# Performance work log

Hardware: AMD Instinct MI355X
Metric: run time of the kernel (lower is better)

Reference implementation:

```python
import jax, jax.numpy as jnp
import numpy as np

N_NODES = 32768
N_EDGES = 524288
IN_CH = 128
OUT_CH = 128
EDGE_CH = 64
HIDDEN = 128


def setup_inputs() -> dict:
    key = jax.random.key(0)
    ks = jax.random.split(key, 8)
    x = jax.random.normal(ks[0], (N_NODES, IN_CH), dtype=jnp.float32)
    edge_index = jax.random.randint(ks[1], (2, N_EDGES), 0, N_NODES, dtype=jnp.int64)
    edge_attr = jax.random.uniform(ks[2], (N_EDGES, EDGE_CH), dtype=jnp.float32)
    # filter_network: Linear(edge_ch, hidden) -> tanh -> Linear(hidden, out)
    s1 = 1.0 / np.sqrt(EDGE_CH)
    s2 = 1.0 / np.sqrt(HIDDEN)
    W1 = jax.random.uniform(ks[3], (EDGE_CH, HIDDEN), jnp.float32, -s1, s1)
    b1 = jax.random.uniform(ks[4], (HIDDEN,), jnp.float32, -s1, s1)
    W2 = jax.random.uniform(ks[5], (HIDDEN, OUT_CH), jnp.float32, -s2, s2)
    b2 = jax.random.uniform(ks[6], (OUT_CH,), jnp.float32, -s2, s2)
    # attention_vector [out, 1], xavier_uniform with gain 1.414
    lim = 1.414 * np.sqrt(6.0 / (OUT_CH + 1))
    attn = jax.random.uniform(ks[7], (OUT_CH,), jnp.float32, -lim, lim)
    return {"x": x, "edge_index": edge_index, "edge_attr": edge_attr,
            "W1": W1, "b1": b1, "W2": W2, "b2": b2, "attn": attn}


def _segment_softmax(scores, segment_ids, num_segments):
    # PyG-style numerically stable softmax over segments
    seg_max = jax.ops.segment_max(scores, segment_ids, num_segments=num_segments)
    seg_max = jnp.where(jnp.isfinite(seg_max), seg_max, 0.0)
    e = jnp.exp(scores - seg_max[segment_ids])
    denom = jax.ops.segment_sum(e, segment_ids, num_segments=num_segments)
    return e / (denom[segment_ids] + 1e-16)


def reference(x, edge_index, edge_attr, W1, b1, W2, b2, attn):
    source, target = edge_index[0], edge_index[1]
    n_nodes = x.shape[0]
    source_features = x[source]                                  # [E, in]
    edge_attr_norm = edge_attr / (jnp.linalg.norm(edge_attr, axis=-1, keepdims=True) + 1e-8)
    h = jnp.tanh(edge_attr_norm @ W1 + b1)                       # [E, hidden]
    edge_filters = h @ W2 + b2                                   # [E, out]
    messages = source_features * edge_filters                    # [E, out]
    attention_scores = messages @ attn                           # [E]
    attention_weights = _segment_softmax(attention_scores, target, n_nodes)
    messages = messages * attention_weights[:, None]
    output = jax.ops.segment_sum(messages, target, num_segments=n_nodes)  # [N, out]
    return output, attention_weights
```

## Files before the change

### kernel.cpp

```cpp
#include <hip/hip_runtime.h>
#include <stdint.h>

typedef short short8 __attribute__((ext_vector_type(8)));
typedef float f32x16 __attribute__((ext_vector_type(16)));
typedef unsigned ux4 __attribute__((ext_vector_type(4)));

__device__ __forceinline__ unsigned cvtpk(float lo, float hi){
  unsigned r;
  asm("v_cvt_pk_bf16_f32 %0, %1, %2" : "=v"(r) : "v"(lo), "v"(hi));
  return r;
}

__device__ __forceinline__ short8 frag_from(unsigned a, unsigned b, unsigned c, unsigned d){
  union { unsigned u[4]; short8 s; } t;
  t.u[0] = a; t.u[1] = b; t.u[2] = c; t.u[3] = d;
  return t.s;
}

__global__ void k_setup(const float* __restrict__ x, uint2* __restrict__ xb, int n4,
                        const int* __restrict__ ei, int* __restrict__ rowptr, int E,
                        const float* __restrict__ W1, const float* __restrict__ W2,
                        ux4* __restrict__ Wf)
{
  const long long tid = (long long)blockIdx.x * 256 + threadIdx.x;
  if (tid < 48 * 64) {
    const int f = (int)(tid >> 6), l = (int)(tid & 63);
    const int r = l & 31, hh = l >> 5;
    float v[8];
    if (f < 16) {
      const int mf = f >> 2, ks = f & 3;
      const int c = 32 * mf + r, kb = ks * 16 + hh * 8;
#pragma unroll
      for (int j = 0; j < 8; ++j) v[j] = W1[(kb + j) * 128 + c];
    } else {
      const int f2 = f - 16, mf2 = f2 >> 3, ks = f2 & 7;
      const int o = 32 * mf2 + r, cb = ks * 16 + hh * 8;
#pragma unroll
      for (int j = 0; j < 8; ++j) v[j] = W2[(cb + j) * 128 + o];
    }
    ux4 d;
    d.x = cvtpk(v[0], v[1]); d.y = cvtpk(v[2], v[3]);
    d.z = cvtpk(v[4], v[5]); d.w = cvtpk(v[6], v[7]);
    Wf[(long long)f * 64 + l] = d;
  }
  const long long tot = (n4 > E) ? n4 : E;
  for (long long i = tid; i < tot; i += (long long)gridDim.x * 256) {
    if (i < n4) {
      float4 v = ((const float4*)x)[i];
      uint2 o; o.x = cvtpk(v.x, v.y); o.y = cvtpk(v.z, v.w);
      xb[i] = o;
    }
    if (i < E) atomicAdd(&rowptr[ei[E + i]], 1);
  }
}

__global__ __launch_bounds__(1024)
void k_scan(int* __restrict__ p, int N){
  __shared__ int ls[1024];
  const int t = threadIdx.x;
  const int chunk = (N + 1023) >> 10;
  const int c0 = t * chunk, c1 = min(N, c0 + chunk);
  int s = 0;
  for (int i = c0; i < c1; ++i) s += p[i];
  ls[t] = s;
  __syncthreads();
  for (int off = 1; off < 1024; off <<= 1) {
    int add = (t >= off) ? ls[t - off] : 0;
    __syncthreads();
    ls[t] += add;
    __syncthreads();
  }
  int run = (t == 0) ? 0 : ls[t - 1];
  for (int i = c0; i < c1; ++i) { int v = p[i]; p[i] = run; run += v; }
}

__global__ void k_fill(const int* __restrict__ ei, int* __restrict__ rowptr,
                       int* __restrict__ pose, int* __restrict__ eidx, int E){
  for (long long i = (long long)blockIdx.x * 256 + threadIdx.x; i < E;
       i += (long long)gridDim.x * 256) {
    int tg = ei[E + i];
    int pos = atomicAdd(&rowptr[tg], 1);
    if (pose) pose[i] = pos;
    eidx[pos] = (int)i;
  }
}

#define K1B 512
__global__ __launch_bounds__(K1B)
void k1_fused(const unsigned* __restrict__ xb, const int* __restrict__ ei,
              const float* __restrict__ ea, const ux4* __restrict__ Wf,
              const float* __restrict__ b1, const float* __restrict__ b2,
              const float* __restrict__ attn, const int* __restrict__ eidx,
              unsigned* __restrict__ msgp, float* __restrict__ scoreS, int E)
{
  __shared__ ux4 sWf[48 * 64];
  for (int i = threadIdx.x; i < 48 * 64; i += K1B) sWf[i] = Wf[i];
  __syncthreads();

  const int lane = threadIdx.x & 63;
  const int wv   = threadIdx.x >> 6;
  const int h    = lane >> 5;
  const int r31  = lane & 31;
  const long long gstep = (long long)gridDim.x * (K1B / 64) * 32;
  long long p = ((long long)blockIdx.x * (K1B / 64) + wv) * 32 + r31;
  if (p - r31 >= E) return;

  int eC = eidx[(p < E) ? p : (long long)(E - 1)];
  int srcC = ei[eC];
  unsigned ebC[4][4]; float rinC;
  {
    const float* er = ea + (long long)eC * 64 + h * 8;
    float4 v[8];
#pragma unroll
    for (int ks = 0; ks < 4; ++ks) {
      v[2*ks]   = *(const float4*)(er + ks * 16);
      v[2*ks+1] = *(const float4*)(er + ks * 16 + 4);
    }
    float ss = 0.f;
#pragma unroll
    for (int k8 = 0; k8 < 8; ++k8) {
      ss = fmaf(v[k8].x, v[k8].x, ss); ss = fmaf(v[k8].y, v[k8].y, ss);
      ss = fmaf(v[k8].z, v[k8].z, ss); ss = fmaf(v[k8].w, v[k8].w, ss);
    }
    ss += __shfl_xor(ss, 32);
    rinC = 1.0f / (sqrtf(ss) + 1e-8f);
#pragma unroll
    for (int ks = 0; ks < 4; ++ks) {
      ebC[ks][0] = cvtpk(v[2*ks].x,   v[2*ks].y);
      ebC[ks][1] = cvtpk(v[2*ks].z,   v[2*ks].w);
      ebC[ks][2] = cvtpk(v[2*ks+1].x, v[2*ks+1].y);
      ebC[ks][3] = cvtpk(v[2*ks+1].z, v[2*ks+1].w);
    }
  }
  long long pn = p + gstep;
  bool hasN = (pn - r31) < E;
  int eN = 0;
  if (hasN) eN = eidx[(pn < E) ? pn : (long long)(E - 1)];

  while (true) {
    float4 eaN[8]; int srcN = 0;
    if (hasN) {
      srcN = ei[eN];
      const float* er = ea + (long long)eN * 64 + h * 8;
#pragma unroll
      for (int ks = 0; ks < 4; ++ks) {
        eaN[2*ks]   = *(const float4*)(er + ks * 16);
        eaN[2*ks+1] = *(const float4*)(er + ks * 16 + 4);
      }
    }
    long long pnn = pn + gstep;
    bool hasNN = hasN && ((pnn - r31) < E);
    int eNN = 0;
    if (hasNN) eNN = eidx[(pnn < E) ? pnn : (long long)(E - 1)];

    const unsigned* xrow = xb + (long long)srcC * 64;
    uint2 xw[4];
#pragma unroll
    for (int rq = 0; rq < 4; ++rq)
      xw[rq] = *(const uint2*)(xrow + (8*rq + 4*h) / 2);
    asm volatile("" ::: "memory");

    unsigned hb[8][4];
#pragma unroll
    for (int mf = 0; mf < 4; ++mf) {
      f32x16 a1;
#pragma unroll
      for (int i = 0; i < 16; ++i) a1[i] = 0.f;
#pragma unroll
      for (int ks = 0; ks < 4; ++ks) {
        ux4 w = sWf[(mf * 4 + ks) * 64 + lane];
        a1 = __builtin_amdgcn_mfma_f32_32x32x16_bf16(
            frag_from(w.x, w.y, w.z, w.w),
            frag_from(ebC[ks][0], ebC[ks][1], ebC[ks][2], ebC[ks][3]), a1, 0, 0, 0);
      }
      float hv[16];
#pragma unroll
      for (int rq = 0; rq < 4; ++rq) {
        float4 bc = *(const float4*)(b1 + 32*mf + 8*rq + 4*h);
#pragma unroll
        for (int i = 0; i < 4; ++i) {
          float pre = fmaf(a1[rq*4+i], rinC, ((const float*)&bc)[i]);
          float e2  = __expf(2.0f * pre);
          hv[rq*4+i] = 1.0f - 2.0f / (e2 + 1.0f);
        }
      }
#pragma unroll
      for (int q = 0; q < 2; ++q) {
        unsigned A = cvtpk(hv[q*8+0], hv[q*8+1]);
        unsigned B = cvtpk(hv[q*8+2], hv[q*8+3]);
        unsigned C = cvtpk(hv[q*8+4], hv[q*8+5]);
        unsigned D = cvtpk(hv[q*8+6], hv[q*8+7]);
        unsigned Axr = (unsigned)__shfl_xor((int)A, 32);
        unsigned Bxr = (unsigned)__shfl_xor((int)B, 32);
        unsigned Cxr = (unsigned)__shfl_xor((int)C, 32);
        unsigned Dxr = (unsigned)__shfl_xor((int)D, 32);
        hb[2*mf+q][0] = h ? Cxr : A;
        hb[2*mf+q][1] = h ? Dxr : B;
        hb[2*mf+q][2] = h ? C   : Axr;
        hb[2*mf+q][3] = h ? D   : Bxr;
      }
    }

    float score = 0.f;
#pragma unroll
    for (int mf2 = 0; mf2 < 4; ++mf2) {
      uint2 xwN[4];
      if (mf2 < 3) {
#pragma unroll
        for (int rq = 0; rq < 4; ++rq)
          xwN[rq] = *(const uint2*)(xrow + (32*(mf2+1) + 8*rq + 4*h) / 2);
      }
      f32x16 a2;
#pragma unroll
      for (int i = 0; i < 16; ++i) a2[i] = 0.f;
#pragma unroll
      for (int ks = 0; ks < 8; ++ks) {
        ux4 w = sWf[(16 + mf2 * 8 + ks) * 64 + lane];
        a2 = __builtin_amdgcn_mfma_f32_32x32x16_bf16(
            frag_from(w.x, w.y, w.z, w.w),
            frag_from(hb[ks][0], hb[ks][1], hb[ks][2], hb[ks][3]), a2, 0, 0, 0);
      }
      unsigned pk[8];
#pragma unroll
      for (int rq = 0; rq < 4; ++rq) {
        const int o0 = 32*mf2 + 8*rq + 4*h;
        float4 b2c = *(const float4*)(b2 + o0);
        float4 atc = *(const float4*)(attn + o0);
        float x0 = __uint_as_float(xw[rq].x << 16);
        float x1 = __uint_as_float(xw[rq].x & 0xffff0000u);
        float x2 = __uint_as_float(xw[rq].y << 16);
        float x3 = __uint_as_float(xw[rq].y & 0xffff0000u);
        float m0 = (a2[rq*4+0] + b2c.x) * x0;
        float m1 = (a2[rq*4+1] + b2c.y) * x1;
        float m2 = (a2[rq*4+2] + b2c.z) * x2;
        float m3 = (a2[rq*4+3] + b2c.w) * x3;
        score = fmaf(m0, atc.x, score);
        score = fmaf(m1, atc.y, score);
        score = fmaf(m2, atc.z, score);
        score = fmaf(m3, atc.w, score);
        pk[2*rq]   = cvtpk(m0, m1);
        pk[2*rq+1] = cvtpk(m2, m3);
      }
      if (p < E) {
        ux4* dst = (ux4*)(msgp + p * 64 + 16*mf2 + 8*h);
        ux4 s0, s1;
        s0.x = pk[0]; s0.y = pk[1]; s0.z = pk[2]; s0.w = pk[3];
        s1.x = pk[4]; s1.y = pk[5]; s1.z = pk[6]; s1.w = pk[7];
        dst[0] = s0; dst[1] = s1;
      }
      if (mf2 < 3) {
#pragma unroll
        for (int rq = 0; rq < 4; ++rq) xw[rq] = xwN[rq];
      }
    }
    score += __shfl_xor(score, 32);
    if (h == 0 && p < E) scoreS[p] = score;

    if (!hasN) break;
    float ss = 0.f;
#pragma unroll
    for (int k8 = 0; k8 < 8; ++k8) {
      ss = fmaf(eaN[k8].x, eaN[k8].x, ss); ss = fmaf(eaN[k8].y, eaN[k8].y, ss);
      ss = fmaf(eaN[k8].z, eaN[k8].z, ss); ss = fmaf(eaN[k8].w, eaN[k8].w, ss);
    }
    ss += __shfl_xor(ss, 32);
    rinC = 1.0f / (sqrtf(ss) + 1e-8f);
#pragma unroll
    for (int ks = 0; ks < 4; ++ks) {
      ebC[ks][0] = cvtpk(eaN[2*ks].x,   eaN[2*ks].y);
      ebC[ks][1] = cvtpk(eaN[2*ks].z,   eaN[2*ks].w);
      ebC[ks][2] = cvtpk(eaN[2*ks+1].x, eaN[2*ks+1].y);
      ebC[ks][3] = cvtpk(eaN[2*ks+1].z, eaN[2*ks+1].w);
    }
    srcC = srcN; p = pn; pn = pnn; hasN = hasNN; eN = eNN;
  }
}

template<int FUSEW>
__global__ __launch_bounds__(256)
void k_gather(const unsigned* __restrict__ msgp, const float* __restrict__ scoreS,
              const int* __restrict__ rowptr, const int* __restrict__ eidx,
              float* __restrict__ lse, float* __restrict__ wreg,
              float* __restrict__ out, int N)
{
  const int lane = threadIdx.x & 63;
  const int node = blockIdx.x * 4 + (threadIdx.x >> 6);
  if (node >= N) return;
  const int end   = rowptr[node];
  const int start = node ? rowptr[node - 1] : 0;
  const int L     = end - start;

  if (L <= 64) {
    float sc = (lane < L) ? scoreS[start + lane] : -3.4e38f;
    float mn = sc;
#pragma unroll
    for (int off = 32; off; off >>= 1) mn = fmaxf(mn, __shfl_xor(mn, off));
    float ex = (lane < L) ? __expf(sc - mn) : 0.f;
    float s = ex;
#pragma unroll
    for (int off = 32; off; off >>= 1) s += __shfl_xor(s, off);
    const float w = ex / (s + 1e-16f);
    if (FUSEW) {
      if (lane < L) wreg[eidx[start + lane]] = w;
    } else if (lane == 0) {
      lse[node] = mn + logf(s + 1e-16f);
    }

    const int g = lane & 15;
    const int q = lane >> 4;
    float acc8[8];
#pragma unroll
    for (int i = 0; i < 8; ++i) acc8[i] = 0.f;
    const int nit = (L + 3) >> 2;
#pragma unroll 2
    for (int it = 0; it < nit; ++it) {
      const int r = 4 * it + q;
      const float wj = __shfl(w, r);
      ux4 md = *(const ux4*)(msgp + (long long)(start + r) * 64 + 4 * g);
#pragma unroll
      for (int k = 0; k < 4; ++k) {
        const unsigned u = ((const unsigned*)&md)[k];
        acc8[2*k]   = fmaf(wj, __uint_as_float(u << 16),          acc8[2*k]);
        acc8[2*k+1] = fmaf(wj, __uint_as_float(u & 0xffff0000u), acc8[2*k+1]);
      }
    }
#pragma unroll
    for (int i = 0; i < 8; ++i) {
      acc8[i] += __shfl_xor(acc8[i], 16);
      acc8[i] += __shfl_xor(acc8[i], 32);
    }
    if (lane < 16) {
#pragma unroll
      for (int k = 0; k < 4; ++k) {
        const int u = 4 * lane + k;
        const int ch0 = 32*(u >> 4) + 8*((u >> 1) & 3) + 4*((u >> 3) & 1) + 2*(u & 1);
        float2 o; o.x = acc8[2*k]; o.y = acc8[2*k+1];
        *(float2*)(out + (long long)node * 128 + ch0) = o;
      }
    }
    return;
  }

  float2 acc; acc.x = 0.f; acc.y = 0.f;
  float m = -3.4e38f, s = 0.f;
  for (int c0 = 0; c0 < L; c0 += 64) {
    const int j = c0 + lane;
    float sc = (j < L) ? scoreS[start + j] : -3.4e38f;
    float cm = sc;
#pragma unroll
    for (int off = 32; off; off >>= 1) cm = fmaxf(cm, __shfl_xor(cm, off));
    const float mn = fmaxf(m, cm);
    float ex = (j < L) ? __expf(sc - mn) : 0.f;
#pragma unroll
    for (int off = 32; off; off >>= 1) ex += __shfl_xor(ex, off);
    s = s * __expf(m - mn) + ex;
    m = mn;
  }
  const float lsev = m + logf(s + 1e-16f);
  if (!FUSEW && lane == 0) lse[node] = lsev;

  for (int c0 = 0; c0 < L; c0 += 64) {
    const int j = c0 + lane;
    float w = (j < L) ? __expf(scoreS[start + j] - lsev) : 0.f;
    if (FUSEW && j < L) wreg[eidx[start + j]] = w;
    const int jn = min(64, L - c0);
#pragma unroll 4
    for (int j2 = 0; j2 < jn; ++j2) {
      float wj = __shfl(w, j2);
      unsigned md = msgp[(long long)(start + c0 + j2) * 64 + lane];
      acc.x = fmaf(wj, __uint_as_float(md << 16),          acc.x);
      acc.y = fmaf(wj, __uint_as_float(md & 0xffff0000u), acc.y);
    }
  }
  const int mf2 = lane >> 4, hh = (lane >> 3) & 1, rq = (lane >> 1) & 3, half = lane & 1;
  const int ch0 = 32*mf2 + 8*rq + 4*hh + 2*half;
  *(float2*)(out + (long long)node * 128 + ch0) = acc;
}

__global__ void k_wfin(int* __restrict__ pw, const int* __restrict__ ei,
                       const float* __restrict__ scoreS, const float* __restrict__ lse,
                       int E){
  for (long long i = (long long)blockIdx.x * 256 + threadIdx.x; i < E;
       i += (long long)gridDim.x * 256) {
    int pos = pw[i];
    float w = __expf(scoreS[pos] - lse[ei[E + i]]);
    pw[i] = __float_as_int(w);
  }
}

extern "C" void kernel_launch(void* const* d_in, const int* in_sizes, int n_in,
                              void* d_out, int out_size, void* d_ws, size_t ws_size,
                              hipStream_t stream)
{
  const float* x    = (const float*)d_in[0];
  const int*   ei   = (const int*)d_in[1];
  const float* ea   = (const float*)d_in[2];
  const float* W1   = (const float*)d_in[3];
  const float* b1   = (const float*)d_in[4];
  const float* W2   = (const float*)d_in[5];
  const float* b2   = (const float*)d_in[6];
  const float* attn = (const float*)d_in[7];
  const int N = in_sizes[0] / 128;
  const int E = in_sizes[2] / 64;
  if (E <= 0 || N <= 0) return;

  float* out   = (float*)d_out;
  float* wregN = out + (long long)N * 128;
  ux4*     Wf     = (ux4*)d_out;
  size_t   offE   = 65536;
  int*     eidxDO = (int*)((char*)d_out + offE);
  size_t   offX   = (offE + (size_t)E * 4 + 255) & ~(size_t)255;
  unsigned* xb    = (unsigned*)((char*)d_out + offX);

  char* wsb = (char*)d_ws;
  unsigned* msgp   = (unsigned*)wsb;
  float*    scoreS = (float*)(wsb + (size_t)E * 256);
  int*      rowptr = (int*)(wsb + (size_t)E * 260);
  float*    lse    = (float*)(wsb + (size_t)E * 260 + (size_t)N * 4);
  int*      eidxWS = (int*)(wsb + (size_t)E * 260 + (size_t)N * 8);
  const size_t need1 = (size_t)E * 260 + (size_t)N * 8;
  const size_t need2 = need1 + (size_t)E * 4;
  if (ws_size < need1) return;
  if ((size_t)out_size < (size_t)N * 128 + (size_t)E) return;
  if ((size_t)N * 512 < offX + (size_t)N * 256) return;

  const bool fused = (ws_size >= need2);
  int* eidx = fused ? eidxWS : eidxDO;

  (void)hipMemsetAsync(rowptr, 0, (size_t)N * 4, stream);
  k_setup<<<1024, 256, 0, stream>>>(x, (uint2*)xb, N * 32, ei, rowptr, E, W1, W2, Wf);
  k_scan<<<1, 1024, 0, stream>>>(rowptr, N);
  k_fill<<<1024, 256, 0, stream>>>(ei, rowptr, fused ? nullptr : (int*)wregN, eidx, E);
  const long long nwaves = ((long long)E + 31) / 32;
  const int grid = (int)min((long long)512, (nwaves + (K1B/64) - 1) / (K1B/64));
  k1_fused<<<grid, K1B, 0, stream>>>(xb, ei, ea, Wf, b1, b2, attn,
                                     eidx, msgp, scoreS, E);
  if (fused) {
    k_gather<1><<<(N + 3) / 4, 256, 0, stream>>>(msgp, scoreS, rowptr, eidx,
                                                 lse, wregN, out, N);
  } else {
    k_gather<0><<<(N + 3) / 4, 256, 0, stream>>>(msgp, scoreS, rowptr, eidx,
                                                 lse, wregN, out, N);
    k_wfin<<<1024, 256, 0, stream>>>((int*)wregN, ei, scoreS, lse, E);
  }
}
```

Baseline: 261.4 us.

## Merge all stages into one cooperative persistent kernel with grid syncs

Replaces the memset, setup, single-block scan, fill, fused message, and gather launches with one cooperative kernel that moves between phases using grid-wide syncs. The scan becomes a two-level multi-block scan instead of one 1024-thread block, and the weight fragments are built straight into shared memory. This is meant to remove launch gaps and the serial scan bottleneck. In exchange, the grid is capped by occupancy at no more than 512 blocks, the gather phase now runs on this fixed grid instead of one block per four nodes, and host-side device-property and occupancy queries are added to every call.

```diff
diff --git a/kernel.cpp b/kernel.cpp
--- a/kernel.cpp
+++ b/kernel.cpp
@@ -1,5 +1,8 @@
 #include <hip/hip_runtime.h>
+#include <hip/hip_cooperative_groups.h>
 #include <stdint.h>
+
+namespace cg = cooperative_groups;
 
 typedef short short8 __attribute__((ext_vector_type(8)));
 typedef float f32x16 __attribute__((ext_vector_type(16)));
@@ -17,14 +20,36 @@
   return t.s;
 }
 
-__global__ void k_setup(const float* __restrict__ x, uint2* __restrict__ xb, int n4,
-                        const int* __restrict__ ei, int* __restrict__ rowptr, int E,
-                        const float* __restrict__ W1, const float* __restrict__ W2,
-                        ux4* __restrict__ Wf)
+struct SM {
+  ux4 wf[3072];
+  int scan[512];
+};
+
+#define MBLK 512
+
+__global__ __launch_bounds__(MBLK, 4)
+void k_mega(const float* __restrict__ x, const int* __restrict__ ei,
+            const float* __restrict__ ea, const float* __restrict__ W1,
+            const float* __restrict__ b1, const float* __restrict__ W2,
+            const float* __restrict__ b2, const float* __restrict__ attn,
+            unsigned* __restrict__ xb, int* __restrict__ eidx,
+            unsigned* __restrict__ msgp, float* __restrict__ scoreS,
+            int* __restrict__ rowptr, int* __restrict__ bsum,
+            float* __restrict__ wreg, float* __restrict__ out, int N, int E)
 {
-  const long long tid = (long long)blockIdx.x * 256 + threadIdx.x;
-  if (tid < 48 * 64) {
-    const int f = (int)(tid >> 6), l = (int)(tid & 63);
+  cg::grid_group g = cg::this_grid();
+  __shared__ SM sm;
+
+  const int tix  = threadIdx.x;
+  const int lane = tix & 63;
+  const int wv   = tix >> 6;
+  const int h    = lane >> 5;
+  const int r31  = lane & 31;
+  const long long gsz = (long long)gridDim.x * MBLK;
+  const long long gt  = (long long)blockIdx.x * MBLK + tix;
+
+  for (int t = tix; t < 3072; t += MBLK) {
+    const int f = t >> 6, l = t & 63;
     const int r = l & 31, hh = l >> 5;
     float v[8];
     if (f < 16) {
@@ -41,350 +66,330 @@
     ux4 d;
     d.x = cvtpk(v[0], v[1]); d.y = cvtpk(v[2], v[3]);
     d.z = cvtpk(v[4], v[5]); d.w = cvtpk(v[6], v[7]);
-    Wf[(long long)f * 64 + l] = d;
-  }
-  const long long tot = (n4 > E) ? n4 : E;
-  for (long long i = tid; i < tot; i += (long long)gridDim.x * 256) {
-    if (i < n4) {
+    sm.wf[t] = d;
+  }
+  for (long long i = gt; i < N; i += gsz) rowptr[i] = 0;
+  {
+    const long long n4 = (long long)N * 32;
+    for (long long i = gt; i < n4; i += gsz) {
       float4 v = ((const float4*)x)[i];
       uint2 o; o.x = cvtpk(v.x, v.y); o.y = cvtpk(v.z, v.w);
-      xb[i] = o;
-    }
-    if (i < E) atomicAdd(&rowptr[ei[E + i]], 1);
-  }
-}
-
-__global__ __launch_bounds__(1024)
-void k_scan(int* __restrict__ p, int N){
-  __shared__ int ls[1024];
-  const int t = threadIdx.x;
-  const int chunk = (N + 1023) >> 10;
-  const int c0 = t * chunk, c1 = min(N, c0 + chunk);
-  int s = 0;
-  for (int i = c0; i < c1; ++i) s += p[i];
-  ls[t] = s;
-  __syncthreads();
-  for (int off = 1; off < 1024; off <<= 1) {
-    int add = (t >= off) ? ls[t - off] : 0;
+      ((uint2*)xb)[i] = o;
+    }
+  }
+  g.sync();
+
+  for (long long i = gt; i < E; i += gsz)
+    atomicAdd(&rowptr[ei[E + i]], 1);
+  g.sync();
+
+  {
+    const int B   = gridDim.x;
+    const int npb = (N + B - 1) / B;
+    const int npt = (npb + MBLK - 1) / MBLK;
+    const int base = blockIdx.x * npb;
+    const int lim  = min(base + npb, N);
+    const int i0 = base + tix * npt;
+    const int i1 = min(lim, i0 + npt);
+    int s = 0;
+    for (int i = i0; i < i1; ++i) s += rowptr[i];
+    sm.scan[tix] = s;
     __syncthreads();
-    ls[t] += add;
-    __syncthreads();
-  }
-  int run = (t == 0) ? 0 : ls[t - 1];
-  for (int i = c0; i < c1; ++i) { int v = p[i]; p[i] = run; run += v; }
-}
-
-__global__ void k_fill(const int* __restrict__ ei, int* __restrict__ rowptr,
-                       int* __restrict__ pose, int* __restrict__ eidx, int E){
-  for (long long i = (long long)blockIdx.x * 256 + threadIdx.x; i < E;
-       i += (long long)gridDim.x * 256) {
+    for (int off = 1; off < MBLK; off <<= 1) {
+      int add = (tix >= off) ? sm.scan[tix - off] : 0;
+      __syncthreads();
+      sm.scan[tix] += add;
+      __syncthreads();
+    }
+    int run = tix ? sm.scan[tix - 1] : 0;
+    for (int i = i0; i < i1; ++i) { int v = rowptr[i]; rowptr[i] = run; run += v; }
+    if (tix == MBLK - 1) bsum[blockIdx.x] = sm.scan[MBLK - 1];
+    g.sync();
+    if (blockIdx.x == 0) {
+      int v = (tix < B) ? bsum[tix] : 0;
+      sm.scan[tix] = v;
+      __syncthreads();
+      for (int off = 1; off < MBLK; off <<= 1) {
+        int add = (tix >= off) ? sm.scan[tix - off] : 0;
+        __syncthreads();
+        sm.scan[tix] += add;
+        __syncthreads();
+      }
+      if (tix < B) bsum[tix] = tix ? sm.scan[tix - 1] : 0;
+    }
+    g.sync();
+    const int add = bsum[blockIdx.x];
+    if (add) for (int i = i0; i < i1; ++i) rowptr[i] += add;
+  }
+  g.sync();
+
+  for (long long i = gt; i < E; i += gsz) {
     int tg = ei[E + i];
     int pos = atomicAdd(&rowptr[tg], 1);
-    if (pose) pose[i] = pos;
     eidx[pos] = (int)i;
   }
-}
-
-#define K1B 512
-__global__ __launch_bounds__(K1B)
-void k1_fused(const unsigned* __restrict__ xb, const int* __restrict__ ei,
-              const float* __restrict__ ea, const ux4* __restrict__ Wf,
-              const float* __restrict__ b1, const float* __restrict__ b2,
-              const float* __restrict__ attn, const int* __restrict__ eidx,
-              unsigned* __restrict__ msgp, float* __restrict__ scoreS, int E)
-{
-  __shared__ ux4 sWf[48 * 64];
-  for (int i = threadIdx.x; i < 48 * 64; i += K1B) sWf[i] = Wf[i];
-  __syncthreads();
-
-  const int lane = threadIdx.x & 63;
-  const int wv   = threadIdx.x >> 6;
-  const int h    = lane >> 5;
-  const int r31  = lane & 31;
-  const long long gstep = (long long)gridDim.x * (K1B / 64) * 32;
-  long long p = ((long long)blockIdx.x * (K1B / 64) + wv) * 32 + r31;
-  if (p - r31 >= E) return;
-
-  int eC = eidx[(p < E) ? p : (long long)(E - 1)];
-  int srcC = ei[eC];
-  unsigned ebC[4][4]; float rinC;
+  g.sync();
+
   {
-    const float* er = ea + (long long)eC * 64 + h * 8;
-    float4 v[8];
-#pragma unroll
-    for (int ks = 0; ks < 4; ++ks) {
-      v[2*ks]   = *(const float4*)(er + ks * 16);
-      v[2*ks+1] = *(const float4*)(er + ks * 16 + 4);
-    }
-    float ss = 0.f;
-#pragma unroll
-    for (int k8 = 0; k8 < 8; ++k8) {
-      ss = fmaf(v[k8].x, v[k8].x, ss); ss = fmaf(v[k8].y, v[k8].y, ss);
-      ss = fmaf(v[k8].z, v[k8].z, ss); ss = fmaf(v[k8].w, v[k8].w, ss);
-    }
-    ss += __shfl_xor(ss, 32);
-    rinC = 1.0f / (sqrtf(ss) + 1e-8f);
-#pragma unroll
-    for (int ks = 0; ks < 4; ++ks) {
-      ebC[ks][0] = cvtpk(v[2*ks].x,   v[2*ks].y);
-      ebC[ks][1] = cvtpk(v[2*ks].z,   v[2*ks].w);
-      ebC[ks][2] = cvtpk(v[2*ks+1].x, v[2*ks+1].y);
-      ebC[ks][3] = cvtpk(v[2*ks+1].z, v[2*ks+1].w);
-    }
-  }
-  long long pn = p + gstep;
-  bool hasN = (pn - r31) < E;
-  int eN = 0;
-  if (hasN) eN = eidx[(pn < E) ? pn : (long long)(E - 1)];
-
-  while (true) {
-    float4 eaN[8]; int srcN = 0;
-    if (hasN) {
-      srcN = ei[eN];
-      const float* er = ea + (long long)eN * 64 + h * 8;
-#pragma unroll
-      for (int ks = 0; ks < 4; ++ks) {
-        eaN[2*ks]   = *(const float4*)(er + ks * 16);
-        eaN[2*ks+1] = *(const float4*)(er + ks * 16 + 4);
-      }
-    }
-    long long pnn = pn + gstep;
-    bool hasNN = hasN && ((pnn - r31) < E);
-    int eNN = 0;
-    if (hasNN) eNN = eidx[(pnn < E) ? pnn : (long long)(E - 1)];
-
-    const unsigned* xrow = xb + (long long)srcC * 64;
-    uint2 xw[4];
-#pragma unroll
-    for (int rq = 0; rq < 4; ++rq)
-      xw[rq] = *(const uint2*)(xrow + (8*rq + 4*h) / 2);
-    asm volatile("" ::: "memory");
-
-    unsigned hb[8][4];
-#pragma unroll
-    for (int mf = 0; mf < 4; ++mf) {
-      f32x16 a1;
-#pragma unroll
-      for (int i = 0; i < 16; ++i) a1[i] = 0.f;
-#pragma unroll
-      for (int ks = 0; ks < 4; ++ks) {
-        ux4 w = sWf[(mf * 4 + ks) * 64 + lane];
-        a1 = __builtin_amdgcn_mfma_f32_32x32x16_bf16(
-            frag_from(w.x, w.y, w.z, w.w),
-            frag_from(ebC[ks][0], ebC[ks][1], ebC[ks][2], ebC[ks][3]), a1, 0, 0, 0);
-      }
-      float hv[16];
-#pragma unroll
-      for (int rq = 0; rq < 4; ++rq) {
-        float4 bc = *(const float4*)(b1 + 32*mf + 8*rq + 4*h);
-#pragma unroll
-        for (int i = 0; i < 4; ++i) {
-          float pre = fmaf(a1[rq*4+i], rinC, ((const float*)&bc)[i]);
-          float e2  = __expf(2.0f * pre);
-          hv[rq*4+i] = 1.0f - 2.0f / (e2 + 1.0f);
-        }
-      }
-#pragma unroll
-      for (int q = 0; q < 2; ++q) {
-        unsigned A = cvtpk(hv[q*8+0], hv[q*8+1]);
-        unsigned B = cvtpk(hv[q*8+2], hv[q*8+3]);
-        unsigned C = cvtpk(hv[q*8+4], hv[q*8+5]);
-        unsigned D = cvtpk(hv[q*8+6], hv[q*8+7]);
-        unsigned Axr = (unsigned)__shfl_xor((int)A, 32);
-        unsigned Bxr = (unsigned)__shfl_xor((int)B, 32);
-        unsigned Cxr = (unsigned)__shfl_xor((int)C, 32);
-        unsigned Dxr = (unsigned)__shfl_xor((int)D, 32);
-        hb[2*mf+q][0] = h ? Cxr : A;
-        hb[2*mf+q][1] = h ? Dxr : B;
-        hb[2*mf+q][2] = h ? C   : Axr;
-        hb[2*mf+q][3] = h ? D   : Bxr;
-      }
-    }
-
-    float score = 0.f;
-#pragma unroll
-    for (int mf2 = 0; mf2 < 4; ++mf2) {
-      uint2 xwN[4];
-      if (mf2 < 3) {
+    const long long gstep = (long long)gridDim.x * (MBLK / 64) * 32;
+    long long p = ((long long)blockIdx.x * (MBLK / 64) + wv) * 32 + r31;
+    if (p - r31 < E) {
+      int eC = eidx[(p < E) ? p : (long long)(E - 1)];
+      int srcC = ei[eC];
+      unsigned ebC[4][4]; float rinC;
+      {
+        const float* er = ea + (long long)eC * 64 + h * 8;
+        float4 v[8];
+#pragma unroll
+        for (int ks = 0; ks < 4; ++ks) {
+          v[2*ks]   = *(const float4*)(er + ks * 16);
+          v[2*ks+1] = *(const float4*)(er + ks * 16 + 4);
+        }
+        float ss = 0.f;
+#pragma unroll
+        for (int k8 = 0; k8 < 8; ++k8) {
+          ss = fmaf(v[k8].x, v[k8].x, ss); ss = fmaf(v[k8].y, v[k8].y, ss);
+          ss = fmaf(v[k8].z, v[k8].z, ss); ss = fmaf(v[k8].w, v[k8].w, ss);
+        }
+        ss += __shfl_xor(ss, 32);
+        rinC = 1.0f / (sqrtf(ss) + 1e-8f);
+#pragma unroll
+        for (int ks = 0; ks < 4; ++ks) {
+          ebC[ks][0] = cvtpk(v[2*ks].x,   v[2*ks].y);
+          ebC[ks][1] = cvtpk(v[2*ks].z,   v[2*ks].w);
+          ebC[ks][2] = cvtpk(v[2*ks+1].x, v[2*ks+1].y);
+          ebC[ks][3] = cvtpk(v[2*ks+1].z, v[2*ks+1].w);
+        }
+      }
+      long long pn = p + gstep;
+      bool hasN = (pn - r31) < E;
+      int eN = 0;
+      if (hasN) eN = eidx[(pn < E) ? pn : (long long)(E - 1)];
+
+      while (true) {
+        float4 eaN[8]; int srcN = 0;
+        if (hasN) {
+          srcN = ei[eN];
+          const float* er = ea + (long long)eN * 64 + h * 8;
+#pragma unroll
+          for (int ks = 0; ks < 4; ++ks) {
+            eaN[2*ks]   = *(const float4*)(er + ks * 16);
+            eaN[2*ks+1] = *(const float4*)(er + ks * 16 + 4);
+          }
+        }
+        long long pnn = pn + gstep;
+        bool hasNN = hasN && ((pnn - r31) < E);
+        int eNN = 0;
+        if (hasNN) eNN = eidx[(pnn < E) ? pnn : (long long)(E - 1)];
+
+        const unsigned* xrow = xb + (long long)srcC * 64;
+        uint2 xw[4];
 #pragma unroll
         for (int rq = 0; rq < 4; ++rq)
-          xwN[rq] = *(const uint2*)(xrow + (32*(mf2+1) + 8*rq + 4*h) / 2);
-      }
-      f32x16 a2;
-#pragma unroll
-      for (int i = 0; i < 16; ++i) a2[i] = 0.f;
-#pragma unroll
-      for (int ks = 0; ks < 8; ++ks) {
-        ux4 w = sWf[(16 + mf2 * 8 + ks) * 64 + lane];
-        a2 = __builtin_amdgcn_mfma_f32_32x32x16_bf16(
-            frag_from(w.x, w.y, w.z, w.w),
-            frag_from(hb[ks][0], hb[ks][1], hb[ks][2], hb[ks][3]), a2, 0, 0, 0);
-      }
-      unsigned pk[8];
-#pragma unroll
-      for (int rq = 0; rq < 4; ++rq) {
-        const int o0 = 32*mf2 + 8*rq + 4*h;
-        float4 b2c = *(const float4*)(b2 + o0);
-        float4 atc = *(const float4*)(attn + o0);
-        float x0 = __uint_as_float(xw[rq].x << 16);
-        float x1 = __uint_as_float(xw[rq].x & 0xffff0000u);
-        float x2 = __uint_as_float(xw[rq].y << 16);
-        float x3 = __uint_as_float(xw[rq].y & 0xffff0000u);
-        float m0 = (a2[rq*4+0] + b2c.x) * x0;
-        float m1 = (a2[rq*4+1] + b2c.y) * x1;
-        float m2 = (a2[rq*4+2] + b2c.z) * x2;
-        float m3 = (a2[rq*4+3] + b2c.w) * x3;
-        score = fmaf(m0, atc.x, score);
-        score = fmaf(m1, atc.y, score);
-        score = fmaf(m2, atc.z, score);
-        score = fmaf(m3, atc.w, score);
-        pk[2*rq]   = cvtpk(m0, m1);
-        pk[2*rq+1] = cvtpk(m2, m3);
-      }
-      if (p < E) {
-        ux4* dst = (ux4*)(msgp + p * 64 + 16*mf2 + 8*h);
-        ux4 s0, s1;
-        s0.x = pk[0]; s0.y = pk[1]; s0.z = pk[2]; s0.w = pk[3];
-        s1.x = pk[4]; s1.y = pk[5]; s1.z = pk[6]; s1.w = pk[7];
-        dst[0] = s0; dst[1] = s1;
-      }
-      if (mf2 < 3) {
-#pragma unroll
-        for (int rq = 0; rq < 4; ++rq) xw[rq] = xwN[rq];
-      }
-    }
-    score += __shfl_xor(score, 32);
-    if (h == 0 && p < E) scoreS[p] = score;
-
-    if (!hasN) break;
-    float ss = 0.f;
-#pragma unroll
-    for (int k8 = 0; k8 < 8; ++k8) {
-      ss = fmaf(eaN[k8].x, eaN[k8].x, ss); ss = fmaf(eaN[k8].y, eaN[k8].y, ss);
-      ss = fmaf(eaN[k8].z, eaN[k8].z, ss); ss = fmaf(eaN[k8].w, eaN[k8].w, ss);
-    }
-    ss += __shfl_xor(ss, 32);
-    rinC = 1.0f / (sqrtf(ss) + 1e-8f);
-#pragma unroll
-    for (int ks = 0; ks < 4; ++ks) {
-      ebC[ks][0] = cvtpk(eaN[2*ks].x,   eaN[2*ks].y);
-      ebC[ks][1] = cvtpk(eaN[2*ks].z,   eaN[2*ks].w);
-      ebC[ks][2] = cvtpk(eaN[2*ks+1].x, eaN[2*ks+1].y);
-      ebC[ks][3] = cvtpk(eaN[2*ks+1].z, eaN[2*ks+1].w);
-    }
-    srcC = srcN; p = pn; pn = pnn; hasN = hasNN; eN = eNN;
-  }
-}
-
-template<int FUSEW>
-__global__ __launch_bounds__(256)
-void k_gather(const unsigned* __restrict__ msgp, const float* __restrict__ scoreS,
-              const int* __restrict__ rowptr, const int* __restrict__ eidx,
-              float* __restrict__ lse, float* __restrict__ wreg,
-              float* __restrict__ out, int N)
-{
-  const int lane = threadIdx.x & 63;
-  const int node = blockIdx.x * 4 + (threadIdx.x >> 6);
-  if (node >= N) return;
-  const int end   = rowptr[node];
-  const int start = node ? rowptr[node - 1] : 0;
-  const int L     = end - start;
-
-  if (L <= 64) {
-    float sc = (lane < L) ? scoreS[start + lane] : -3.4e38f;
-    float mn = sc;
-#pragma unroll
-    for (int off = 32; off; off >>= 1) mn = fmaxf(mn, __shfl_xor(mn, off));
-    float ex = (lane < L) ? __expf(sc - mn) : 0.f;
-    float s = ex;
-#pragma unroll
-    for (int off = 32; off; off >>= 1) s += __shfl_xor(s, off);
-    const float w = ex / (s + 1e-16f);
-    if (FUSEW) {
+          xw[rq] = *(const uint2*)(xrow + (8*rq + 4*h) / 2);
+        asm volatile("" ::: "memory");
+
+        unsigned hb[8][4];
+#pragma unroll
+        for (int mf = 0; mf < 4; ++mf) {
+          f32x16 a1;
+#pragma unroll
+          for (int i = 0; i < 16; ++i) a1[i] = 0.f;
+#pragma unroll
+          for (int ks = 0; ks < 4; ++ks) {
+            ux4 w = sm.wf[(mf * 4 + ks) * 64 + lane];
+            a1 = __builtin_amdgcn_mfma_f32_32x32x16_bf16(
+                frag_from(w.x, w.y, w.z, w.w),
+                frag_from(ebC[ks][0], ebC[ks][1], ebC[ks][2], ebC[ks][3]), a1, 0, 0, 0);
+          }
+          float hv[16];
+#pragma unroll
+          for (int rq = 0; rq < 4; ++rq) {
+            float4 bc = *(const float4*)(b1 + 32*mf + 8*rq + 4*h);
+#pragma unroll
+            for (int i = 0; i < 4; ++i) {
+              float pre = fmaf(a1[rq*4+i], rinC, ((const float*)&bc)[i]);
+              float e2  = __expf(2.0f * pre);
+              hv[rq*4+i] = 1.0f - 2.0f / (e2 + 1.0f);
+            }
+          }
+#pragma unroll
+          for (int q = 0; q < 2; ++q) {
+            unsigned A = cvtpk(hv[q*8+0], hv[q*8+1]);
+            unsigned B = cvtpk(hv[q*8+2], hv[q*8+3]);
+            unsigned C = cvtpk(hv[q*8+4], hv[q*8+5]);
+            unsigned D = cvtpk(hv[q*8+6], hv[q*8+7]);
+            unsigned Axr = (unsigned)__shfl_xor((int)A, 32);
+            unsigned Bxr = (unsigned)__shfl_xor((int)B, 32);
+            unsigned Cxr = (unsigned)__shfl_xor((int)C, 32);
+            unsigned Dxr = (unsigned)__shfl_xor((int)D, 32);
+            hb[2*mf+q][0] = h ? Cxr : A;
+            hb[2*mf+q][1] = h ? Dxr : B;
+            hb[2*mf+q][2] = h ? C   : Axr;
+            hb[2*mf+q][3] = h ? D   : Bxr;
+          }
+        }
+
+        float score = 0.f;
+#pragma unroll
+        for (int mf2 = 0; mf2 < 4; ++mf2) {
+          uint2 xwN[4];
+          if (mf2 < 3) {
+#pragma unroll
+            for (int rq = 0; rq < 4; ++rq)
+              xwN[rq] = *(const uint2*)(xrow + (32*(mf2+1) + 8*rq + 4*h) / 2);
+          }
+          f32x16 a2;
+#pragma unroll
+          for (int i = 0; i < 16; ++i) a2[i] = 0.f;
+#pragma unroll
+          for (int ks = 0; ks < 8; ++ks) {
+            ux4 w = sm.wf[(16 + mf2 * 8 + ks) * 64 + lane];
+            a2 = __builtin_amdgcn_mfma_f32_32x32x16_bf16(
+                frag_from(w.x, w.y, w.z, w.w),
+                frag_from(hb[ks][0], hb[ks][1], hb[ks][2], hb[ks][3]), a2, 0, 0, 0);
+          }
+          unsigned pk[8];
+#pragma unroll
+          for (int rq = 0; rq < 4; ++rq) {
+            const int o0 = 32*mf2 + 8*rq + 4*h;
+            float4 b2c = *(const float4*)(b2 + o0);
+            float4 atc = *(const float4*)(attn + o0);
+            float x0 = __uint_as_float(xw[rq].x << 16);
+            float x1 = __uint_as_float(xw[rq].x & 0xffff0000u);
+            float x2 = __uint_as_float(xw[rq].y << 16);
+            float x3 = __uint_as_float(xw[rq].y & 0xffff0000u);
+            float m0 = (a2[rq*4+0] + b2c.x) * x0;
+            float m1 = (a2[rq*4+1] + b2c.y) * x1;
+            float m2 = (a2[rq*4+2] + b2c.z) * x2;
+            float m3 = (a2[rq*4+3] + b2c.w) * x3;
+            score = fmaf(m0, atc.x, score);
+            score = fmaf(m1, atc.y, score);
+            score = fmaf(m2, atc.z, score);
+            score = fmaf(m3, atc.w, score);
+            pk[2*rq]   = cvtpk(m0, m1);
+            pk[2*rq+1] = cvtpk(m2, m3);
+          }
+          if (p < E) {
+            ux4* dst = (ux4*)(msgp + p * 64 + 16*mf2 + 8*h);
+            ux4 s0, s1;
+            s0.x = pk[0]; s0.y = pk[1]; s0.z = pk[2]; s0.w = pk[3];
+            s1.x = pk[4]; s1.y = pk[5]; s1.z = pk[6]; s1.w = pk[7];
+            dst[0] = s0; dst[1] = s1;
+          }
+          if (mf2 < 3) {
+#pragma unroll
+            for (int rq = 0; rq < 4; ++rq) xw[rq] = xwN[rq];
+          }
+        }
+        score += __shfl_xor(score, 32);
+        if (h == 0 && p < E) scoreS[p] = score;
+
+        if (!hasN) break;
+        float ss = 0.f;
+#pragma unroll
+        for (int k8 = 0; k8 < 8; ++k8) {
+          ss = fmaf(eaN[k8].x, eaN[k8].x, ss); ss = fmaf(eaN[k8].y, eaN[k8].y, ss);
+          ss = fmaf(eaN[k8].z, eaN[k8].z, ss); ss = fmaf(eaN[k8].w, eaN[k8].w, ss);
+        }
+        ss += __shfl_xor(ss, 32);
+        rinC = 1.0f / (sqrtf(ss) + 1e-8f);
+#pragma unroll
+        for (int ks = 0; ks < 4; ++ks) {
+          ebC[ks][0] = cvtpk(eaN[2*ks].x,   eaN[2*ks].y);
+          ebC[ks][1] = cvtpk(eaN[2*ks].z,   eaN[2*ks].w);
+          ebC[ks][2] = cvtpk(eaN[2*ks+1].x, eaN[2*ks+1].y);
+          ebC[ks][3] = cvtpk(eaN[2*ks+1].z, eaN[2*ks+1].w);
+        }
+        srcC = srcN; p = pn; pn = pnn; hasN = hasNN; eN = eNN;
+      }
+    }
+  }
+  g.sync();
+
+  for (int node = blockIdx.x * 8 + wv; node < N; node += gridDim.x * 8) {
+    const int end   = rowptr[node];
+    const int start = node ? rowptr[node - 1] : 0;
+    const int L     = end - start;
+
+    if (L <= 64) {
+      float sc = (lane < L) ? scoreS[start + lane] : -3.4e38f;
+      float mn = sc;
+#pragma unroll
+      for (int off = 32; off; off >>= 1) mn = fmaxf(mn, __shfl_xor(mn, off));
+      float ex = (lane < L) ? __expf(sc - mn) : 0.f;
+      float s = ex;
+#pragma unroll
+      for (int off = 32; off; off >>= 1) s += __shfl_xor(s, off);
+      const float w = ex / (s + 1e-16f);
       if (lane < L) wreg[eidx[start + lane]] = w;
-    } else if (lane == 0) {
-      lse[node] = mn + logf(s + 1e-16f);
-    }
-
-    const int g = lane & 15;
-    const int q = lane >> 4;
-    float acc8[8];
-#pragma unroll
-    for (int i = 0; i < 8; ++i) acc8[i] = 0.f;
-    const int nit = (L + 3) >> 2;
+
+      const int gq = lane & 15;
+      const int q  = lane >> 4;
+      float acc8[8];
+#pragma unroll
+      for (int i = 0; i < 8; ++i) acc8[i] = 0.f;
+      const int nit = (L + 3) >> 2;
 #pragma unroll 2
-    for (int it = 0; it < nit; ++it) {
-      const int r = 4 * it + q;
-      const float wj = __shfl(w, r);
-      ux4 md = *(const ux4*)(msgp + (long long)(start + r) * 64 + 4 * g);
-#pragma unroll
-      for (int k = 0; k < 4; ++k) {
-        const unsigned u = ((const unsigned*)&md)[k];
-        acc8[2*k]   = fmaf(wj, __uint_as_float(u << 16),          acc8[2*k]);
-        acc8[2*k+1] = fmaf(wj, __uint_as_float(u & 0xffff0000u), acc8[2*k+1]);
-      }
-    }
-#pragma unroll
-    for (int i = 0; i < 8; ++i) {
-      acc8[i] += __shfl_xor(acc8[i], 16);
-      acc8[i] += __shfl_xor(acc8[i], 32);
-    }
-    if (lane < 16) {
-#pragma unroll
-      for (int k = 0; k < 4; ++k) {
-        const int u = 4 * lane + k;
-        const int ch0 = 32*(u >> 4) + 8*((u >> 1) & 3) + 4*((u >> 3) & 1) + 2*(u & 1);
-        float2 o; o.x = acc8[2*k]; o.y = acc8[2*k+1];
-        *(float2*)(out + (long long)node * 128 + ch0) = o;
-      }
-    }
-    return;
-  }
-
-  float2 acc; acc.x = 0.f; acc.y = 0.f;
-  float m = -3.4e38f, s = 0.f;
-  for (int c0 = 0; c0 < L; c0 += 64) {
-    const int j = c0 + lane;
-    float sc = (j < L) ? scoreS[start + j] : -3.4e38f;
-    float cm = sc;
-#pragma unroll
-    for (int off = 32; off; off >>= 1) cm = fmaxf(cm, __shfl_xor(cm, off));
-    const float mn = fmaxf(m, cm);
-    float ex = (j < L) ? __expf(sc - mn) : 0.f;
-#pragma unroll
-    for (int off = 32; off; off >>= 1) ex += __shfl_xor(ex, off);
-    s = s * __expf(m - mn) + ex;
-    m = mn;
-  }
-  const float lsev = m + logf(s + 1e-16f);
-  if (!FUSEW && lane == 0) lse[node] = lsev;
-
-  for (int c0 = 0; c0 < L; c0 += 64) {
-    const int j = c0 + lane;
-    float w = (j < L) ? __expf(scoreS[start + j] - lsev) : 0.f;
-    if (FUSEW && j < L) wreg[eidx[start + j]] = w;
-    const int jn = min(64, L - c0);
+      for (int it = 0; it < nit; ++it) {
+        const int r = 4 * it + q;
+        const float wj = __shfl(w, r);
+        ux4 md = *(const ux4*)(msgp + (long long)(start + r) * 64 + 4 * gq);
+#pragma unroll
+        for (int k = 0; k < 4; ++k) {
+          const unsigned u = ((const unsigned*)&md)[k];
+          acc8[2*k]   = fmaf(wj, __uint_as_float(u << 16),          acc8[2*k]);
+          acc8[2*k+1] = fmaf(wj, __uint_as_float(u & 0xffff0000u), acc8[2*k+1]);
+        }
+      }
+#pragma unroll
+      for (int i = 0; i < 8; ++i) {
+        acc8[i] += __shfl_xor(acc8[i], 16);
+        acc8[i] += __shfl_xor(acc8[i], 32);
+      }
+      if (lane < 16) {
+#pragma unroll
+        for (int k = 0; k < 4; ++k) {
+          const int u = 4 * lane + k;
+          const int ch0 = 32*(u >> 4) + 8*((u >> 1) & 3) + 4*((u >> 3) & 1) + 2*(u & 1);
+          float2 o; o.x = acc8[2*k]; o.y = acc8[2*k+1];
+          *(float2*)(out + (long long)node * 128 + ch0) = o;
+        }
+      }
+    } else {
+      float2 acc; acc.x = 0.f; acc.y = 0.f;
+      float m = -3.4e38f, s = 0.f;
+      for (int c0 = 0; c0 < L; c0 += 64) {
+        const int j = c0 + lane;
+        float sc = (j < L) ? scoreS[start + j] : -3.4e38f;
+        float cm = sc;
+#pragma unroll
+        for (int off = 32; off; off >>= 1) cm = fmaxf(cm, __shfl_xor(cm, off));
+        const float mn = fmaxf(m, cm);
+        float ex = (j < L) ? __expf(sc - mn) : 0.f;
+#pragma unroll
+        for (int off = 32; off; off >>= 1) ex += __shfl_xor(ex, off);
+        s = s * __expf(m - mn) + ex;
+        m = mn;
+      }
+      const float inv = 1.0f / (s + 1e-16f);
+      for (int c0 = 0; c0 < L; c0 += 64) {
+        const int j = c0 + lane;
+        float w = (j < L) ? __expf(scoreS[start + j] - m) * inv : 0.f;
+        if (j < L) wreg[eidx[start + j]] = w;
+        const int jn = min(64, L - c0);
 #pragma unroll 4
-    for (int j2 = 0; j2 < jn; ++j2) {
-      float wj = __shfl(w, j2);
-      unsigned md = msgp[(long long)(start + c0 + j2) * 64 + lane];
-      acc.x = fmaf(wj, __uint_as_float(md << 16),          acc.x);
-      acc.y = fmaf(wj, __uint_as_float(md & 0xffff0000u), acc.y);
-    }
-  }
-  const int mf2 = lane >> 4, hh = (lane >> 3) & 1, rq = (lane >> 1) & 3, half = lane & 1;
-  const int ch0 = 32*mf2 + 8*rq + 4*hh + 2*half;
-  *(float2*)(out + (long long)node * 128 + ch0) = acc;
-}
-
-__global__ void k_wfin(int* __restrict__ pw, const int* __restrict__ ei,
-                       const float* __restrict__ scoreS, const float* __restrict__ lse,
-                       int E){
-  for (long long i = (long long)blockIdx.x * 256 + threadIdx.x; i < E;
-       i += (long long)gridDim.x * 256) {
-    int pos = pw[i];
-    float w = __expf(scoreS[pos] - lse[ei[E + i]]);
-    pw[i] = __float_as_int(w);
+        for (int j2 = 0; j2 < jn; ++j2) {
+          float wj = __shfl(w, j2);
+          unsigned md = msgp[(long long)(start + c0 + j2) * 64 + lane];
+          acc.x = fmaf(wj, __uint_as_float(md << 16),          acc.x);
+          acc.y = fmaf(wj, __uint_as_float(md & 0xffff0000u), acc.y);
+        }
+      }
+      const int mf2 = lane >> 4, hh = (lane >> 3) & 1, rq = (lane >> 1) & 3, half = lane & 1;
+      const int ch0 = 32*mf2 + 8*rq + 4*hh + 2*half;
+      *(float2*)(out + (long long)node * 128 + ch0) = acc;
+    }
   }
 }
 
@@ -404,43 +409,37 @@
   const int E = in_sizes[2] / 64;
   if (E <= 0 || N <= 0) return;
 
-  float* out   = (float*)d_out;
-  float* wregN = out + (long long)N * 128;
-  ux4*     Wf     = (ux4*)d_out;
-  size_t   offE   = 65536;
-  int*     eidxDO = (int*)((char*)d_out + offE);
-  size_t   offX   = (offE + (size_t)E * 4 + 255) & ~(size_t)255;
-  unsigned* xb    = (unsigned*)((char*)d_out + offX);
+  float* out  = (float*)d_out;
+  float* wreg = out + (long long)N * 128;
+  unsigned* xb = (unsigned*)d_out;
 
   char* wsb = (char*)d_ws;
   unsigned* msgp   = (unsigned*)wsb;
   float*    scoreS = (float*)(wsb + (size_t)E * 256);
   int*      rowptr = (int*)(wsb + (size_t)E * 260);
-  float*    lse    = (float*)(wsb + (size_t)E * 260 + (size_t)N * 4);
-  int*      eidxWS = (int*)(wsb + (size_t)E * 260 + (size_t)N * 8);
-  const size_t need1 = (size_t)E * 260 + (size_t)N * 8;
-  const size_t need2 = need1 + (size_t)E * 4;
-  if (ws_size < need1) return;
+  int*      bsum   = (int*)(wsb + (size_t)E * 260 + (size_t)N * 4);
+  int*      eidx   = (int*)(wsb + (size_t)E * 260 + (size_t)N * 4 + 4096);
+  const size_t need = (size_t)E * 264 + (size_t)N * 4 + 4096;
+  if (ws_size < need) return;
   if ((size_t)out_size < (size_t)N * 128 + (size_t)E) return;
-  if ((size_t)N * 512 < offX + (size_t)N * 256) return;
-
-  const bool fused = (ws_size >= need2);
-  int* eidx = fused ? eidxWS : eidxDO;
-
-  (void)hipMemsetAsync(rowptr, 0, (size_t)N * 4, stream);
-  k_setup<<<1024, 256, 0, stream>>>(x, (uint2*)xb, N * 32, ei, rowptr, E, W1, W2, Wf);
-  k_scan<<<1, 1024, 0, stream>>>(rowptr, N);
-  k_fill<<<1024, 256, 0, stream>>>(ei, rowptr, fused ? nullptr : (int*)wregN, eidx, E);
-  const long long nwaves = ((long long)E + 31) / 32;
-  const int grid = (int)min((long long)512, (nwaves + (K1B/64) - 1) / (K1B/64));
-  k1_fused<<<grid, K1B, 0, stream>>>(xb, ei, ea, Wf, b1, b2, attn,
-                                     eidx, msgp, scoreS, E);
-  if (fused) {
-    k_gather<1><<<(N + 3) / 4, 256, 0, stream>>>(msgp, scoreS, rowptr, eidx,
-                                                 lse, wregN, out, N);
-  } else {
-    k_gather<0><<<(N + 3) / 4, 256, 0, stream>>>(msgp, scoreS, rowptr, eidx,
-                                                 lse, wregN, out, N);
-    k_wfin<<<1024, 256, 0, stream>>>((int*)wregN, ei, scoreS, lse, E);
-  }
+  if ((size_t)N * 512 < (size_t)N * 256) return;
+
+  int dev = 0;
+  (void)hipGetDevice(&dev);
+  hipDeviceProp_t prop;
+  (void)hipGetDeviceProperties(&prop, dev);
+  int occ = 0;
+  (void)hipOccupancyMaxActiveBlocksPerMultiprocessor(
+      &occ, reinterpret_cast<const void*>(&k_mega), MBLK, 0);
+  if (occ < 1) occ = 1;
+  long long grid = (long long)prop.multiProcessorCount * occ;
+  if (grid > 512) grid = 512;
+  if (grid < 1) grid = 1;
+
+  void* args[] = { (void*)&x, (void*)&ei, (void*)&ea, (void*)&W1, (void*)&b1,
+                   (void*)&W2, (void*)&b2, (void*)&attn, (void*)&xb, (void*)&eidx,
+                   (void*)&msgp, (void*)&scoreS, (void*)&rowptr, (void*)&bsum,
+                   (void*)&wreg, (void*)&out, (void*)&N, (void*)&E };
+  (void)hipLaunchCooperativeKernel(reinterpret_cast<const void*>(&k_mega),
+                                   dim3((unsigned)grid), dim3(MBLK), args, 0, stream);
 }
```

New measurement: 651.9 us. +149.3%, slower.
